# Kernel optimization log

Hardware: AMD Instinct MI355X
Metric: run time of the kernel (lower is better)

The kernel has to match this reference:

```python
import jax, jax.numpy as jnp
import numpy as np

WH, WW = 4, 4
N_TOK = WH * WW  # 16
NUM_HEADS = 8
DIM = 96
HEAD_DIM = DIM // NUM_HEADS
SCALE = HEAD_DIM ** -0.5


def _relative_position_index():
    # Faithful to TF: tf.meshgrid default indexing='xy' (same as np.meshgrid default)
    coords = np.stack(np.meshgrid(np.arange(WH), np.arange(WW)))  # [2, WW, WH]
    flat = coords.reshape(2, -1)                                   # [2, N]
    rel = flat[:, :, None] - flat[:, None, :]                      # [2, N, N]
    rel = rel.transpose(1, 2, 0) + np.array([WH - 1, WW - 1])
    rel = rel * np.array([2 * WW - 1, 1])
    return jnp.asarray(rel.sum(-1), dtype=jnp.int32)               # [N, N]

REL_IDX = _relative_position_index()


def setup_inputs() -> dict:
    key = jax.random.key(0)
    ks = jax.random.split(key, 7)
    B, L = 16, 3136
    return {
        "x": jax.random.normal(ks[0], (B, L, N_TOK, DIM), jnp.float32),
        "mask": jax.random.normal(ks[1], (L, N_TOK, N_TOK), jnp.float32),
        "qkv_kernel": jax.random.normal(ks[2], (DIM, 3 * DIM), jnp.float32) * 0.02,
        "qkv_bias": jax.random.normal(ks[3], (3 * DIM,), jnp.float32) * 0.02,
        "proj_kernel": jax.random.normal(ks[4], (DIM, DIM), jnp.float32) * 0.02,
        "proj_bias": jax.random.normal(ks[5], (DIM,), jnp.float32) * 0.02,
        "bias_table": jax.random.normal(ks[6], (49, NUM_HEADS), jnp.float32) * 0.02,
    }


def reference(x, mask, qkv_kernel, qkv_bias, proj_kernel, proj_bias, bias_table):
    B, L, N, C = x.shape
    H, D = NUM_HEADS, HEAD_DIM
    qkv = x @ qkv_kernel + qkv_bias                      # [B, L, N, 3C]
    qkv = qkv.reshape(B * L, N, 3, H, D).transpose(2, 0, 3, 1, 4)  # [3, BL, H, N, D]
    q, k, v = qkv[0], qkv[1], qkv[2]
    attn = jnp.einsum('whid,whjd->whij', q * SCALE, k)   # [BL, H, N, N]
    rel_bias = bias_table[REL_IDX.reshape(-1)].reshape(N, N, H).transpose(2, 0, 1)  # [H, N, N]
    attn = attn + rel_bias
    attn = attn.reshape(B, L, H, N, N) + mask[:, None, :, :]        # broadcast over B, heads
    attn = jax.nn.softmax(attn.reshape(B * L, H, N, N), axis=-1)
    out = jnp.einsum('whij,whjd->whid', attn, v)         # [BL, H, N, D]
    out = out.transpose(0, 2, 1, 3).reshape(B, L, N, C)
    return out @ proj_kernel + proj_bias
```

## Files before the change

### kernel.cpp

```cpp
#include <hip/hip_runtime.h>


typedef __attribute__((ext_vector_type(4))) float f32x4;
typedef __attribute__((ext_vector_type(8))) short s16x8;
typedef __attribute__((ext_vector_type(4))) short s16x4;

#define DEV __device__ __forceinline__

DEV short f2bf(float f) {
    union { float f; unsigned int i; } v; v.f = f;
    unsigned int u = v.i;
    u += 0x7FFFu + ((u >> 16) & 1u);
    return (short)(u >> 16);
}
DEV void lds_fence() { asm volatile("s_waitcnt lgkmcnt(0)" ::: "memory"); }

#define LOG2E  1.4426950408889634f
#define QSCALE (0.2886751345948129f * 1.4426950408889634f)
#define LBASE  3136
#define WIN_PER_WAVE 49

#define WQ_OFF   0
#define WQ_SZ    (96*288*2)
#define ZP_OFF   WQ_SZ
#define WAVE_BASE (WQ_SZ + 64)
#define PW_Q     0
#define PW_K     4352
#define PW_V     8704
#define PW_A     14848
#define PW_O     17408
#define PW_STRIDE 20736
#define SMEM_TOTAL (WAVE_BASE + 4*PW_STRIDE)

#define MFMA(a,b,c) __builtin_amdgcn_mfma_f32_16x16x32_bf16((a),(b),(c),0,0,0)

__global__ __launch_bounds__(256, 1)
void winattn_kernel(const float* __restrict__ x,
                    const float* __restrict__ mask,
                    const float* __restrict__ qkvK,
                    const float* __restrict__ qkvB,
                    const float* __restrict__ projK,
                    const float* __restrict__ projB,
                    const float* __restrict__ biasT,
                    float* __restrict__ out)
{
    extern __shared__ __align__(16) char smem[];
    const int tid    = threadIdx.x;
    const int lane   = tid & 63;
    const int waveid = tid >> 6;
    const int mi     = lane & 15;
    const int g      = lane >> 4;

    for (int i = tid; i < SMEM_TOTAL/4; i += 256)
        ((unsigned int*)smem)[i] = 0u;
    __syncthreads();

    for (int e = tid; e < 96*288; e += 256) {
        int k = e / 288, n = e % 288;
        int t = n >> 4, mr = n & 15;
        int kt = k >> 5, gg = (k >> 3) & 3, jj = k & 7;
        int gs = gg ^ ((mr >> 1) & 3);
        int off = (t*3 + kt)*512 + mr*32 + gs*8 + jj;
        ((unsigned short*)(smem + WQ_OFF))[off] = (unsigned short)f2bf(qkvK[e]);
    }
    __syncthreads();

    char* wbuf = smem + WAVE_BASE + waveid*PW_STRIDE;

    s16x8 wp[6][3];
#pragma unroll
    for (int t = 0; t < 6; ++t)
#pragma unroll
        for (int kt = 0; kt < 3; ++kt) {
            s16x8 v;
#pragma unroll
            for (int jj = 0; jj < 8; ++jj)
                v[jj] = f2bf(projK[(kt*32 + g*8 + jj)*96 + t*16 + mi]);
            wp[t][kt] = v;
        }
    f32x4 qb[12];
#pragma unroll
    for (int t = 0; t < 12; ++t) {
        f32x4 v;
#pragma unroll
        for (int r = 0; r < 4; ++r) v[r] = qkvB[t*16 + g*4 + r];
        qb[t] = v;
    }
    float vbias[6];
#pragma unroll
    for (int t = 0; t < 6; ++t) vbias[t] = qkvB[192 + t*16 + mi];
    f32x4 pb[6];
#pragma unroll
    for (int t = 0; t < 6; ++t) {
        f32x4 v;
#pragma unroll
        for (int r = 0; r < 4; ++r) v[r] = projB[t*16 + g*4 + r];
        pb[t] = v;
    }
    f32x4 rb[8];
#pragma unroll
    for (int h = 0; h < 8; ++h) {
        f32x4 v;
#pragma unroll
        for (int r = 0; r < 4; ++r) {
            int i = mi, j = g*4 + r;
            int idx = ((i & 3) - (j & 3) + 3)*7 + ((i >> 2) - (j >> 2) + 3);
            v[r] = biasT[idx*8 + h] * LOG2E;
        }
        rb[h] = v;
    }
    unsigned qkoff[6], voff[6];
#pragma unroll
    for (int t = 0; t < 6; ++t) {
        int f0 = t*16 + g*4;
        qkoff[t] = (unsigned)(mi*272 + (f0/12)*32 + (f0%12)*2);
        int f3 = t*16 + mi;
        voff[t]  = (unsigned)((f3/12)*768 + (f3%12)*48 + g*8);
    }
    const unsigned lane_woff = (unsigned)(mi*64 + ((g ^ ((mi >> 1) & 3)) * 16));

    const int wave_global = blockIdx.x*4 + waveid;
    const int w0 = wave_global * WIN_PER_WAVE;

    for (int it = 0; it < WIN_PER_WAVE; ++it) {
        const int w = w0 + it;
        const float* xw = x + w*1536;

        s16x8 xf[3];
#pragma unroll
        for (int kt = 0; kt < 3; ++kt) {
            f32x4 a = *(const f32x4*)(xw + mi*96 + kt*32 + g*8);
            f32x4 b = *(const f32x4*)(xw + mi*96 + kt*32 + g*8 + 4);
            s16x8 v;
#pragma unroll
            for (int r = 0; r < 4; ++r) { v[r] = f2bf(a[r]); v[4+r] = f2bf(b[r]); }
            xf[kt] = v;
        }

        const int l = w % LBASE;
        f32x4 mk = *(const f32x4*)(mask + l*256 + mi*16 + g*4);
        mk *= LOG2E;

#pragma unroll
        for (int t = 0; t < 12; ++t) {
            f32x4 c = qb[t];
#pragma unroll
            for (int kt = 0; kt < 3; ++kt) {
                s16x8 wf = *(const s16x8*)(smem + WQ_OFF + (t*3 + kt)*1024 + lane_woff);
                c = MFMA(wf, xf[kt], c);
            }
            const float scl = (t < 6) ? QSCALE : 1.0f;
            s16x4 o;
#pragma unroll
            for (int r = 0; r < 4; ++r) o[r] = f2bf(c[r]*scl);
            char* dst = wbuf + ((t < 6) ? PW_Q : PW_K) + qkoff[(t < 6) ? t : (t-6)];
            *(s16x4*)dst = o;
        }
#pragma unroll
        for (int t = 0; t < 6; ++t) {
            f32x4 c = { vbias[t], vbias[t], vbias[t], vbias[t] };
#pragma unroll
            for (int kt = 0; kt < 3; ++kt) {
                s16x8 wf = *(const s16x8*)(smem + WQ_OFF + ((12+t)*3 + kt)*1024 + lane_woff);
                c = MFMA(xf[kt], wf, c);
            }
            s16x4 o;
#pragma unroll
            for (int r = 0; r < 4; ++r) o[r] = f2bf(c[r]);
            *(s16x4*)(wbuf + PW_V + voff[t]) = o;
        }
        lds_fence();

#pragma unroll
        for (int h = 0; h < 8; ++h) {
            const char* qp = (g < 2) ? (wbuf + PW_Q + mi*272 + h*32 + g*16) : (smem + ZP_OFF);
            const char* kp = (g < 2) ? (wbuf + PW_K + mi*272 + h*32 + g*16) : (smem + ZP_OFF);
            s16x8 kf = *(const s16x8*)kp;
            s16x8 qf = *(const s16x8*)qp;
            f32x4 c = rb[h] + mk;
            f32x4 sc = MFMA(kf, qf, c);

            float m = fmaxf(fmaxf(sc[0], sc[1]), fmaxf(sc[2], sc[3]));
            m = fmaxf(m, __shfl_xor(m, 16, 64));
            m = fmaxf(m, __shfl_xor(m, 32, 64));
            float p0 = exp2f(sc[0]-m), p1 = exp2f(sc[1]-m),
                  p2 = exp2f(sc[2]-m), p3 = exp2f(sc[3]-m);
            float s = (p0+p1) + (p2+p3);
            s += __shfl_xor(s, 16, 64);
            s += __shfl_xor(s, 32, 64);
            float rs = 1.0f / s;

            char* ab = wbuf + PW_A + (h & 1)*1280;
            s16x4 av; av[0]=f2bf(p0*rs); av[1]=f2bf(p1*rs); av[2]=f2bf(p2*rs); av[3]=f2bf(p3*rs);
            *(s16x4*)(ab + mi*80 + g*8) = av;
            lds_fence();

            s16x8 af = *(const s16x8*)(ab + mi*80 + g*16);
            const char* vp = (g < 2) ? (wbuf + PW_V + h*768 + mi*48 + g*16) : (smem + ZP_OFF);
            s16x8 vf = *(const s16x8*)vp;
            f32x4 z = {0.f, 0.f, 0.f, 0.f};
            f32x4 oc = MFMA(vf, af, z);
            if (g < 3) {
                s16x4 ov; ov[0]=f2bf(oc[0]); ov[1]=f2bf(oc[1]); ov[2]=f2bf(oc[2]); ov[3]=f2bf(oc[3]);
                *(s16x4*)(wbuf + PW_O + mi*208 + h*24 + g*8) = ov;
            }
        }
        lds_fence();

        s16x8 of[3];
#pragma unroll
        for (int kt = 0; kt < 3; ++kt)
            of[kt] = *(const s16x8*)(wbuf + PW_O + mi*208 + kt*64 + g*16);
        float* op = out + w*1536 + mi*96 + g*4;
#pragma unroll
        for (int t = 0; t < 6; ++t) {
            f32x4 c = pb[t];
            c = MFMA(wp[t][0], of[0], c);
            c = MFMA(wp[t][1], of[1], c);
            c = MFMA(wp[t][2], of[2], c);
            *(f32x4*)(op + t*16) = c;
        }

        __syncthreads();
    }
}

extern "C" void kernel_launch(void* const* d_in, const int* in_sizes, int n_in,
                              void* d_out, int out_size, void* d_ws, size_t ws_size,
                              hipStream_t stream) {
    const float* x     = (const float*)d_in[0];
    const float* mask  = (const float*)d_in[1];
    const float* qkvK  = (const float*)d_in[2];
    const float* qkvB  = (const float*)d_in[3];
    const float* projK = (const float*)d_in[4];
    const float* projB = (const float*)d_in[5];
    const float* biasT = (const float*)d_in[6];

    (void)in_sizes; (void)n_in; (void)out_size; (void)d_ws; (void)ws_size;

    hipFuncSetAttribute((const void*)winattn_kernel,
                        hipFuncAttributeMaxDynamicSharedMemorySize, SMEM_TOTAL);
    winattn_kernel<<<256, 256, SMEM_TOTAL, stream>>>(
        x, mask, qkvK, qkvB, projK, projB, biasT, (float*)d_out);
}
```

Baseline: 780.8 us.

## Prefetch next window's x and mask, batch per-head attention stages, drop block sync

Register-prefetches the next window's x tile and mask row while the current window computes, so global-load latency is hidden behind the MFMA work. The per-head score, softmax and PV loop is split into three batched phases, with a separate probability buffer per head and one LDS fence instead of eight. The V buffer is compacted and padding rows are read from a zero page. The per-iteration __syncthreads is removed because each wave uses only its own LDS region. This raises register and LDS use per wave.

Result: faster. 673.5 us (-13.7%).

```diff
diff --git a/kernel.cpp b/kernel.cpp
--- a/kernel.cpp
+++ b/kernel.cpp
@@ -27,9 +27,9 @@
 #define PW_Q     0
 #define PW_K     4352
 #define PW_V     8704
-#define PW_A     14848
-#define PW_O     17408
-#define PW_STRIDE 20736
+#define PW_A     13312
+#define PW_O     23552
+#define PW_STRIDE 26880
 #define SMEM_TOTAL (WAVE_BASE + 4*PW_STRIDE)
 
 #define MFMA(a,b,c) __builtin_amdgcn_mfma_f32_16x16x32_bf16((a),(b),(c),0,0,0)
@@ -66,6 +66,7 @@
     __syncthreads();
 
     char* wbuf = smem + WAVE_BASE + waveid*PW_STRIDE;
+    const char* zp = smem + ZP_OFF;
 
     s16x8 wp[6][3];
 #pragma unroll
@@ -115,31 +116,48 @@
         int f0 = t*16 + g*4;
         qkoff[t] = (unsigned)(mi*272 + (f0/12)*32 + (f0%12)*2);
         int f3 = t*16 + mi;
-        voff[t]  = (unsigned)((f3/12)*768 + (f3%12)*48 + g*8);
+        voff[t]  = (unsigned)((f3/12)*576 + (f3%12)*48 + g*8);
     }
     const unsigned lane_woff = (unsigned)(mi*64 + ((g ^ ((mi >> 1) & 3)) * 16));
 
     const int wave_global = blockIdx.x*4 + waveid;
     const int w0 = wave_global * WIN_PER_WAVE;
 
+    f32x4 xa[3], xb[3], mraw;
+    {
+        const float* xw = x + w0*1536;
+#pragma unroll
+        for (int kt = 0; kt < 3; ++kt) {
+            xa[kt] = *(const f32x4*)(xw + mi*96 + kt*32 + g*8);
+            xb[kt] = *(const f32x4*)(xw + mi*96 + kt*32 + g*8 + 4);
+        }
+        mraw = *(const f32x4*)(mask + (w0 % LBASE)*256 + mi*16 + g*4);
+    }
+
     for (int it = 0; it < WIN_PER_WAVE; ++it) {
         const int w = w0 + it;
-        const float* xw = x + w*1536;
 
         s16x8 xf[3];
 #pragma unroll
         for (int kt = 0; kt < 3; ++kt) {
-            f32x4 a = *(const f32x4*)(xw + mi*96 + kt*32 + g*8);
-            f32x4 b = *(const f32x4*)(xw + mi*96 + kt*32 + g*8 + 4);
             s16x8 v;
 #pragma unroll
-            for (int r = 0; r < 4; ++r) { v[r] = f2bf(a[r]); v[4+r] = f2bf(b[r]); }
+            for (int r = 0; r < 4; ++r) { v[r] = f2bf(xa[kt][r]); v[4+r] = f2bf(xb[kt][r]); }
             xf[kt] = v;
         }
-
-        const int l = w % LBASE;
-        f32x4 mk = *(const f32x4*)(mask + l*256 + mi*16 + g*4);
+        f32x4 mk = mraw;
         mk *= LOG2E;
+
+        {
+            const int wn = (it + 1 < WIN_PER_WAVE) ? (w + 1) : w;
+            const float* xn = x + wn*1536;
+#pragma unroll
+            for (int kt = 0; kt < 3; ++kt) {
+                xa[kt] = *(const f32x4*)(xn + mi*96 + kt*32 + g*8);
+                xb[kt] = *(const f32x4*)(xn + mi*96 + kt*32 + g*8 + 4);
+            }
+            mraw = *(const f32x4*)(mask + (wn % LBASE)*256 + mi*16 + g*4);
+        }
 
 #pragma unroll
         for (int t = 0; t < 12; ++t) {
@@ -171,32 +189,36 @@
         }
         lds_fence();
 
+        f32x4 sc[8];
 #pragma unroll
         for (int h = 0; h < 8; ++h) {
-            const char* qp = (g < 2) ? (wbuf + PW_Q + mi*272 + h*32 + g*16) : (smem + ZP_OFF);
-            const char* kp = (g < 2) ? (wbuf + PW_K + mi*272 + h*32 + g*16) : (smem + ZP_OFF);
+            const char* qp = (g < 2) ? (wbuf + PW_Q + mi*272 + h*32 + g*16) : zp;
+            const char* kp = (g < 2) ? (wbuf + PW_K + mi*272 + h*32 + g*16) : zp;
             s16x8 kf = *(const s16x8*)kp;
             s16x8 qf = *(const s16x8*)qp;
             f32x4 c = rb[h] + mk;
-            f32x4 sc = MFMA(kf, qf, c);
-
-            float m = fmaxf(fmaxf(sc[0], sc[1]), fmaxf(sc[2], sc[3]));
+            sc[h] = MFMA(kf, qf, c);
+        }
+#pragma unroll
+        for (int h = 0; h < 8; ++h) {
+            float m = fmaxf(fmaxf(sc[h][0], sc[h][1]), fmaxf(sc[h][2], sc[h][3]));
             m = fmaxf(m, __shfl_xor(m, 16, 64));
             m = fmaxf(m, __shfl_xor(m, 32, 64));
-            float p0 = exp2f(sc[0]-m), p1 = exp2f(sc[1]-m),
-                  p2 = exp2f(sc[2]-m), p3 = exp2f(sc[3]-m);
+            float p0 = exp2f(sc[h][0]-m), p1 = exp2f(sc[h][1]-m),
+                  p2 = exp2f(sc[h][2]-m), p3 = exp2f(sc[h][3]-m);
             float s = (p0+p1) + (p2+p3);
             s += __shfl_xor(s, 16, 64);
             s += __shfl_xor(s, 32, 64);
             float rs = 1.0f / s;
-
-            char* ab = wbuf + PW_A + (h & 1)*1280;
             s16x4 av; av[0]=f2bf(p0*rs); av[1]=f2bf(p1*rs); av[2]=f2bf(p2*rs); av[3]=f2bf(p3*rs);
-            *(s16x4*)(ab + mi*80 + g*8) = av;
-            lds_fence();
-
-            s16x8 af = *(const s16x8*)(ab + mi*80 + g*16);
-            const char* vp = (g < 2) ? (wbuf + PW_V + h*768 + mi*48 + g*16) : (smem + ZP_OFF);
+            *(s16x4*)(wbuf + PW_A + h*1280 + mi*80 + g*8) = av;
+        }
+        lds_fence();
+
+#pragma unroll
+        for (int h = 0; h < 8; ++h) {
+            s16x8 af = *(const s16x8*)(wbuf + PW_A + h*1280 + mi*80 + g*16);
+            const char* vp = (g < 2 && mi < 12) ? (wbuf + PW_V + h*576 + mi*48 + g*16) : zp;
             s16x8 vf = *(const s16x8*)vp;
             f32x4 z = {0.f, 0.f, 0.f, 0.f};
             f32x4 oc = MFMA(vf, af, z);
@@ -220,8 +242,6 @@
             c = MFMA(wp[t][2], of[2], c);
             *(f32x4*)(op + t*16) = c;
         }
-
-        __syncthreads();
     }
 }
 
```
